# Optimization experiments

Hardware: AMD Instinct MI355X
Metric: run time of the kernel (lower is better)

## Reference

```python
import jax, jax.numpy as jnp
import numpy as np

HEADS = 8
DIM_HEAD = 64


def setup_inputs() -> dict:
    key = jax.random.key(0)
    ks = jax.random.split(key, 5)
    B, N, C, coor = 2, 2048, 256, 3
    dim_inner = HEADS * DIM_HEAD  # 512
    # weight scale 1/16 ~ 1/sqrt(256) keeps softmax logits in a sane range
    w_scale = 1.0 / 16.0
    return {
        "x": jax.random.normal(ks[0], (B, N, C, coor), dtype=jnp.float32),
        "Wq": jax.random.normal(ks[1], (dim_inner, C), dtype=jnp.float32) * w_scale,
        "Wk": jax.random.normal(ks[2], (dim_inner, C), dtype=jnp.float32) * w_scale,
        "Wv": jax.random.normal(ks[3], (dim_inner, C), dtype=jnp.float32) * w_scale,
        "Wo": jax.random.normal(ks[4], (C, dim_inner), dtype=jnp.float32) * w_scale,
    }


def _split_heads(t, B, N, coor):
    # b n (h d) c -> b h n (d c)
    t = t.reshape(B, N, HEADS, DIM_HEAD, coor)
    t = t.transpose(0, 2, 1, 3, 4)
    return t.reshape(B, HEADS, N, DIM_HEAD * coor)


def reference(x, Wq, Wk, Wv, Wo):
    B, N, C, coor = x.shape
    # VNLinear: einsum('... i c, o i -> ... o c')
    q = jnp.einsum('bnic,oi->bnoc', x, Wq)
    k = jnp.einsum('bnic,oi->bnoc', x, Wk)
    v = jnp.einsum('bnic,oi->bnoc', x, Wv)
    q = _split_heads(q, B, N, coor)  # (B, H, N, d*c)
    k = _split_heads(k, B, N, coor)
    v = _split_heads(v, B, N, coor)
    scale = (DIM_HEAD * coor) ** -0.5
    sim = jnp.einsum('bhie,bhje->bhij', q, k) * scale  # (B, H, N, N)
    attn = jax.nn.softmax(sim, axis=-1)
    out = jnp.einsum('bhij,bhje->bhie', attn, v)  # (B, H, N, d*c)
    # b h n (d c) -> b n (h d) c
    out = out.reshape(B, HEADS, N, DIM_HEAD, coor).transpose(0, 2, 1, 3, 4)
    out = out.reshape(B, N, HEADS * DIM_HEAD, coor)
    # to_out VNLinear
    return jnp.einsum('bnic,oi->bnoc', out, Wo)  # (B, N, C, 3)
```

## Files before the change

### kernel.cpp

```cpp
#include <hip/hip_runtime.h>

#define HEADS 8
#define DH 64
#define CO 3
#define E 192
#define NSEQ 2048
#define BATCH 2
#define CIN 256
#define DINNER 512
#define NTOK 4096
#define BHTOT 16

typedef __attribute__((ext_vector_type(8))) short bf16x8;
typedef __attribute__((ext_vector_type(4))) short bf16x4;
typedef __attribute__((ext_vector_type(4))) float f32x4;

static __device__ inline short f2bf(float f) {
  union { float f; unsigned u; } v; v.f = f;
  unsigned r = (v.u + 0x7FFFu + ((v.u >> 16) & 1u)) >> 16;
  return (short)r;
}

static __device__ inline void load_lds16(const short* g, short* l) {
  __builtin_amdgcn_global_load_lds(
      (const __attribute__((address_space(1))) void*)g,
      (__attribute__((address_space(3))) void*)l, 16, 0, 0);
}


__global__ __launch_bounds__(256) void prep_w(const float* __restrict__ Wq,
                                              const float* __restrict__ Wk,
                                              const float* __restrict__ Wv,
                                              const float* __restrict__ Wo,
                                              short* __restrict__ wqkvp,
                                              short* __restrict__ wop) {
  int idx = blockIdx.x * 256 + threadIdx.x;
  const float qscale = 0.07216878364870323f * 1.4426950408889634f;
  if (idx < 1536 * 256) {
    int o = idx >> 8, i = idx & 255;
    float v;
    if (o < 512) v = Wq[idx] * qscale;
    else if (o < 1024) v = Wk[idx - 512 * 256];
    else v = Wv[idx - 1024 * 256];
    int nt = o >> 4, ln = o & 15, ks = i >> 5, qd = (i >> 3) & 3, j = i & 7;
    wqkvp[((size_t)(nt * 8 + ks)) * 512 + (qd * 16 + ln) * 8 + j] = f2bf(v);
  } else {
    int j0 = idx - 1536 * 256;
    if (j0 < 256 * 512) {
      int o2 = j0 >> 9, i = j0 & 511;
      int nt = o2 >> 4, ln = o2 & 15, ks = i >> 5, qd = (i >> 3) & 3, j = i & 7;
      wop[((size_t)(nt * 16 + ks)) * 512 + (qd * 16 + ln) * 8 + j] = f2bf(Wo[j0]);
    }
  }
}

__global__ __launch_bounds__(256) void prep_x(const float* __restrict__ x,
                                              short* __restrict__ xcp) {
  int idx = blockIdx.x * 256 + threadIdx.x;
  int t = idx >> 8, i = idx & 255;
  const float* p = x + (size_t)idx * 3;
  float a = p[0], b = p[1], c = p[2];
  int mt = t >> 4, ln = t & 15, ks = i >> 5, qd = (i >> 3) & 3, j = i & 7;
  size_t inner = (size_t)(qd * 16 + ln) * 8 + j;
  xcp[((size_t)(0 * 256 + mt) * 8 + ks) * 512 + inner] = f2bf(a);
  xcp[((size_t)(1 * 256 + mt) * 8 + ks) * 512 + inner] = f2bf(b);
  xcp[((size_t)(2 * 256 + mt) * 8 + ks) * 512 + inner] = f2bf(c);
}

__global__ __launch_bounds__(256) void qkv_gemm(const short* __restrict__ xcp,
                                                const short* __restrict__ wqkvp,
                                                short* __restrict__ qp,
                                                short* __restrict__ kp,
                                                short* __restrict__ vp) {
  __shared__ __align__(16) short pool[17408];
  int c = blockIdx.z, ntb = blockIdx.x, mtb = blockIdx.y;
  int tid = threadIdx.x, wave = tid >> 6, lane = tid & 63;
  int ln = lane & 15, quad = lane >> 4;
  int wm = wave >> 1, wn = wave & 1;

  const short* gA = xcp + ((size_t)(c * 256 + mtb * 8) * 8) * 512;
  const short* gB = wqkvp + ((size_t)(ntb * 8) * 8) * 512;

  f32x4 acc[4][4] = {};
#pragma unroll
  for (int i = 0; i < 2; i++) {
    int q = tid + 256 * i, mf = q >> 6, l = q & 63;
    load_lds16(gA + (size_t)(mf * 8) * 512 + l * 8, pool + q * 8);
    load_lds16(gB + (size_t)(mf * 8) * 512 + l * 8, pool + 8192 + q * 8);
  }
  for (int ks = 0; ks < 8; ks++) {
    int b = ks & 1;
    __syncthreads();
    if (ks < 7) {
#pragma unroll
      for (int i = 0; i < 2; i++) {
        int q = tid + 256 * i, mf = q >> 6, l = q & 63;
        load_lds16(gA + (size_t)(mf * 8 + ks + 1) * 512 + l * 8, pool + (b ^ 1) * 4096 + q * 8);
        load_lds16(gB + (size_t)(mf * 8 + ks + 1) * 512 + l * 8, pool + 8192 + (b ^ 1) * 4096 + q * 8);
      }
    }
    const short* As = pool + b * 4096;
    const short* Bs = pool + 8192 + b * 4096;
    bf16x8 af[4], bfr[4];
#pragma unroll
    for (int i = 0; i < 4; i++) af[i] = *(const bf16x8*)&As[(wm * 4 + i) * 512 + lane * 8];
#pragma unroll
    for (int j = 0; j < 4; j++) bfr[j] = *(const bf16x8*)&Bs[(wn * 4 + j) * 512 + lane * 8];
#pragma unroll
    for (int i = 0; i < 4; i++)
#pragma unroll
      for (int j = 0; j < 4; j++)
        acc[i][j] = __builtin_amdgcn_mfma_f32_16x16x32_bf16(af[i], bfr[j], acc[i][j], 0, 0, 0);
  }

  int mat = ntb >> 2;
  int b0 = mtb >> 4;
  if (mat < 2) {
    __syncthreads();
    short* tp = pool;
#pragma unroll
    for (int i = 0; i < 4; i++)
#pragma unroll
      for (int j = 0; j < 4; j++)
#pragma unroll
        for (int jj = 0; jj < 4; jj++)
          tp[(wm * 64 + i * 16 + quad * 4 + jj) * 136 + wn * 64 + j * 16 + ln] =
              f2bf(acc[i][j][jj]);
    __syncthreads();
    short* dst = (mat == 0) ? qp : kp;
    int h0 = (ntb & 3) * 2;
#pragma unroll
    for (int rep = 0; rep < 8; rep++) {
      int gi = rep * 256 + tid;
      int l2 = gi & 15, qd = (gi >> 4) & 3, nf2 = (gi >> 6) & 3,
          esp = (gi >> 8) & 1, hh = (gi >> 9) & 1, kt2 = gi >> 10;
      int tl = kt2 * 64 + nf2 * 16 + l2;
      bf16x8 val = *(const bf16x8*)&tp[tl * 136 + hh * 64 + (esp * 4 + qd) * 8];
      int bhx = b0 * 8 + h0 + hh;
      int kt = (mtb * 2 + kt2) & 31;
      int es = c * 2 + esp;
      size_t off = (((size_t)((bhx * 32 + kt) * 24) + es * 4 + nf2) * 64 +
                    (size_t)(qd * 16 + l2)) * 8;
      *(bf16x8*)(dst + off) = val;
    }
  } else {
#pragma unroll
    for (int i = 0; i < 4; i++) {
      int kt = (mtb * 2 + wm) & 31;
      int ks2 = (i >> 1) & 1;
      int qd2 = (i * 2 + (quad >> 1)) & 3;
#pragma unroll
      for (int j = 0; j < 4; j++) {
        int o = ntb * 128 + wn * 64 + j * 16 + ln;
        int oo = o & 511, h = oo >> 6, d = oo & 63;
        int ef = c * 4 + (d >> 4), l2v = d & 15;
        int bhx = b0 * 8 + h;
        size_t off = ((size_t)((bhx * 32 + kt) * 24 + ks2 * 12 + ef)) * 512 +
                     (qd2 * 16 + l2v) * 8 + (quad & 1) * 4;
        bf16x4 val = { f2bf(acc[i][j][0]), f2bf(acc[i][j][1]),
                       f2bf(acc[i][j][2]), f2bf(acc[i][j][3]) };
        *(bf16x4*)(vp + off) = val;
      }
    }
  }
}

__global__ __launch_bounds__(256, 2) void attn(const short* __restrict__ qp,
                                               const short* __restrict__ kp,
                                               const short* __restrict__ vp,
                                               short* __restrict__ opart,
                                               float* __restrict__ lpart) {
  __shared__ __align__(16) short pool[33792];
  int pair = blockIdx.x, qt = blockIdx.y;
  int bh = pair & 15, kh = pair >> 4;
  int tid = threadIdx.x, wave = tid >> 6, lane = tid & 63;
  int ln = lane & 15, quad = lane >> 4;
  short* Kl = pool;
  short* Vl = pool + 12288;
  short* Pl = pool + 24576;

  bf16x8 qf[2][6];
#pragma unroll
  for (int rg = 0; rg < 2; rg++) {
    int fi = wave * 2 + rg;
    const short* qb = qp +
        ((size_t)(bh * 32 + qt * 2 + (fi >> 2)) * 24 + (fi & 3)) * 512 + lane * 8;
#pragma unroll
    for (int es = 0; es < 6; es++) qf[rg][es] = *(const bf16x8*)(qb + es * 2048);
  }

  float l_r[2][4] = {};
  f32x4 acc[2][12] = {};
  const short* gKb = kp + (size_t)(bh * 32 + kh * 16) * 12288;
  const short* gVb = vp + (size_t)(bh * 32 + kh * 16) * 12288;

  for (int kt = 0; kt < 16; kt++) {
    const short* gK = gKb + (size_t)kt * 12288;
    const short* gV = gVb + (size_t)kt * 12288;
#pragma unroll
    for (int i = 0; i < 6; i++) {
      load_lds16(gK + (i * 256 + tid) * 8, Kl + (i * 256 + tid) * 8);
      load_lds16(gV + (i * 256 + tid) * 8, Vl + (i * 256 + tid) * 8);
    }
    __syncthreads();

    f32x4 s[2][4];
#pragma unroll
    for (int nf = 0; nf < 4; nf++) {
      f32x4 a0 = {}, a1 = {};
#pragma unroll
      for (int es = 0; es < 6; es++) {
        bf16x8 kf = *(const bf16x8*)&Kl[(es * 4 + nf) * 512 + lane * 8];
        a0 = __builtin_amdgcn_mfma_f32_16x16x32_bf16(qf[0][es], kf, a0, 0, 0, 0);
        a1 = __builtin_amdgcn_mfma_f32_16x16x32_bf16(qf[1][es], kf, a1, 0, 0, 0);
      }
      s[0][nf] = a0; s[1][nf] = a1;
    }

#pragma unroll
    for (int rg = 0; rg < 2; rg++)
#pragma unroll
      for (int jj = 0; jj < 4; jj++)
#pragma unroll
        for (int nf = 0; nf < 4; nf++) {
          float p = __builtin_amdgcn_exp2f(s[rg][nf][jj]);
          union { float f; unsigned u; } v; v.f = p;
          Pl[((wave * 2 + rg) * 16 + quad * 4 + jj) * 72 + nf * 16 + ln] =
              (short)((v.u + 0x8000u) >> 16);
          l_r[rg][jj] += p;
        }

    bf16x8 pa[2][2];
#pragma unroll
    for (int rg = 0; rg < 2; rg++) {
      const short* pb = &Pl[((wave * 2 + rg) * 16 + ln) * 72 + quad * 8];
      pa[rg][0] = *(const bf16x8*)pb;
      pa[rg][1] = *(const bf16x8*)(pb + 32);
    }
#pragma unroll
    for (int ef = 0; ef < 12; ef++) {
      bf16x8 v0 = *(const bf16x8*)&Vl[ef * 512 + lane * 8];
      bf16x8 v1 = *(const bf16x8*)&Vl[(12 + ef) * 512 + lane * 8];
#pragma unroll
      for (int rg = 0; rg < 2; rg++) {
        acc[rg][ef] = __builtin_amdgcn_mfma_f32_16x16x32_bf16(pa[rg][0], v0, acc[rg][ef], 0, 0, 0);
        acc[rg][ef] = __builtin_amdgcn_mfma_f32_16x16x32_bf16(pa[rg][1], v1, acc[rg][ef], 0, 0, 0);
      }
    }
    __syncthreads();
  }

#pragma unroll
  for (int rg = 0; rg < 2; rg++)
#pragma unroll
    for (int jj = 0; jj < 4; jj++)
#pragma unroll
      for (int off = 1; off < 16; off <<= 1)
        l_r[rg][jj] += __shfl_xor(l_r[rg][jj], off, 64);

  short* tp = pool;
#pragma unroll
  for (int rg = 0; rg < 2; rg++)
#pragma unroll
    for (int jj = 0; jj < 4; jj++) {
      int row = (wave * 2 + rg) * 16 + quad * 4 + jj;
#pragma unroll
      for (int ef = 0; ef < 12; ef++)
        tp[row * 200 + ef * 16 + ln] = f2bf(acc[rg][ef][jj]);
    }
  __syncthreads();
  const size_t obase = ((size_t)(kh * 16 + bh) * 2048 + qt * 128) * 192;
#pragma unroll
  for (int rep = 0; rep < 12; rep++) {
    int gi = rep * 256 + tid;
    int row = gi / 24, c8 = gi - row * 24;
    *(bf16x8*)(opart + obase + (size_t)row * 192 + c8 * 8) =
        *(const bf16x8*)&tp[row * 200 + c8 * 8];
  }
  int lb = (kh * 16 + bh) * 2048 + qt * 128;
  if (ln == 0) {
#pragma unroll
    for (int rg = 0; rg < 2; rg++)
#pragma unroll
      for (int jj = 0; jj < 4; jj++)
        lpart[lb + (wave * 2 + rg) * 16 + quad * 4 + jj] = l_r[rg][jj];
  }
}

__global__ __launch_bounds__(256) void merge(const short* __restrict__ opart,
                                             const float* __restrict__ lpart,
                                             short* __restrict__ owp) {
  int G = blockIdx.x * 256 + threadIdx.x;
  int inner = G & 63, qd = inner >> 4, row16 = inner & 15;
  int ks = (G >> 6) & 15, h = ks >> 1, esp = ks & 1;
  int mt = (G >> 10) & 255;
  int c = G >> 18;
  int t = mt * 16 + row16, b = t >> 11, n = t & 2047;
  int bh = b * 8 + h;
  size_t so = ((size_t)bh * 2048 + n) * 192 + c * 64 + esp * 32 + qd * 8;
  const size_t HSTR = (size_t)16 * 2048 * 192;
  bf16x8 o1 = *(const bf16x8*)(opart + so);
  bf16x8 o2 = *(const bf16x8*)(opart + HSTR + so);
  float l = lpart[bh * 2048 + n] + lpart[16 * 2048 + bh * 2048 + n];
  float inv = 1.f / l;
  bf16x8 r;
#pragma unroll
  for (int j = 0; j < 8; j++) {
    union { unsigned u; float f; } a, b2;
    a.u = ((unsigned)(unsigned short)o1[j]) << 16;
    b2.u = ((unsigned)(unsigned short)o2[j]) << 16;
    r[j] = f2bf((a.f + b2.f) * inv);
  }
  *(bf16x8*)(owp + (size_t)G * 8) = r;
}

__global__ __launch_bounds__(256) void out_gemm(const short* __restrict__ owp,
                                                const short* __restrict__ wop,
                                                float* __restrict__ out) {
  __shared__ __align__(16) short Al[4096], Bl[2048];
  int c = blockIdx.z, ntb = blockIdx.x, mtb = blockIdx.y;
  int tid = threadIdx.x, wave = tid >> 6, lane = tid & 63;
  int ln = lane & 15, quad = lane >> 4;
  int wm = wave >> 1, wn = wave & 1;

  f32x4 acc[4][2] = {};
  const short* gAb = owp + ((size_t)(c * 256 + mtb * 8) * 16) * 512;
  const short* gBb = wop + ((size_t)(ntb * 4) * 16) * 512;
  for (int ks = 0; ks < 16; ks++) {
#pragma unroll
    for (int i = 0; i < 2; i++) {
      int q = tid + 256 * i, mf = q >> 6, l = q & 63;
      load_lds16(gAb + (size_t)(mf * 16 + ks) * 512 + l * 8, &Al[q * 8]);
    }
    {
      int nf2 = tid >> 6;
      load_lds16(gBb + (size_t)(nf2 * 16 + ks) * 512 + lane * 8, &Bl[tid * 8]);
    }
    __syncthreads();
    bf16x8 af[4], bfr[2];
#pragma unroll
    for (int i = 0; i < 4; i++) af[i] = *(const bf16x8*)&Al[(wm * 4 + i) * 512 + lane * 8];
#pragma unroll
    for (int j = 0; j < 2; j++) bfr[j] = *(const bf16x8*)&Bl[(wn * 2 + j) * 512 + lane * 8];
#pragma unroll
    for (int i = 0; i < 4; i++)
#pragma unroll
      for (int j = 0; j < 2; j++)
        acc[i][j] = __builtin_amdgcn_mfma_f32_16x16x32_bf16(af[i], bfr[j], acc[i][j], 0, 0, 0);
    __syncthreads();
  }
#pragma unroll
  for (int i = 0; i < 4; i++) {
#pragma unroll
    for (int j = 0; j < 2; j++) {
      int o2 = ntb * 64 + (wn * 2 + j) * 16 + ln;
#pragma unroll
      for (int jj = 0; jj < 4; jj++) {
        int t = mtb * 128 + (wm * 4 + i) * 16 + quad * 4 + jj;
        out[((size_t)t * 256 + o2) * 3 + c] = acc[i][j][jj];
      }
    }
  }
}

extern "C" void kernel_launch(void* const* d_in, const int* in_sizes, int n_in,
                              void* d_out, int out_size, void* d_ws, size_t ws_size,
                              hipStream_t stream) {
  const float* x  = (const float*)d_in[0];
  const float* Wq = (const float*)d_in[1];
  const float* Wk = (const float*)d_in[2];
  const float* Wv = (const float*)d_in[3];
  const float* Wo = (const float*)d_in[4];
  float* out = (float*)d_out;

  short* ws    = (short*)d_ws;
  short* xcp   = ws;
  short* wqkvp = xcp + 3 * NTOK * CIN;
  short* wop   = wqkvp + 1536 * 256;
  short* qp    = wop + 256 * 512;
  short* kp    = qp + (size_t)BHTOT * NSEQ * E;
  short* vp    = kp + (size_t)BHTOT * NSEQ * E;
  short* owp   = vp + (size_t)BHTOT * NSEQ * E;
  short* opart = owp + (size_t)3 * NTOK * DINNER;
  float* lpart = (float*)(opart + (size_t)2 * BHTOT * NSEQ * E);

  prep_w<<<2048, 256, 0, stream>>>(Wq, Wk, Wv, Wo, wqkvp, wop);
  prep_x<<<NTOK * CIN / 256, 256, 0, stream>>>(x, xcp);
  qkv_gemm<<<dim3(12, 32, 3), 256, 0, stream>>>(xcp, wqkvp, qp, kp, vp);
  attn<<<dim3(32, 16), 256, 0, stream>>>(qp, kp, vp, opart, lpart);
  merge<<<3072, 256, 0, stream>>>(opart, lpart, owp);
  out_gemm<<<dim3(4, 32, 3), 256, 0, stream>>>(owp, wop, out);
}
```

Measured before the change: 173.6 us.

## Fuse prep kernels, shrink out_gemm tiles, add launch bounds, alias workspace buffers

Merges the weight and input preparation kernels into one launch, which removes a kernel launch. Halves the out_gemm M tile so twice as many blocks run, and adds occupancy hints to qkv_gemm and out_gemm. Reuses workspace by placing lpart over xcp and owp over qp to shrink the memory footprint, which relies on those buffers being dead by the time they are overwritten. Smaller out_gemm tiles load the B operand more often relative to the compute they feed.

New measurement: 170.3 us. Within noise of the previous version (-1.9%).

```diff
diff --git a/kernel.cpp b/kernel.cpp
--- a/kernel.cpp
+++ b/kernel.cpp
@@ -28,13 +28,27 @@
 }
 
 
-__global__ __launch_bounds__(256) void prep_w(const float* __restrict__ Wq,
-                                              const float* __restrict__ Wk,
-                                              const float* __restrict__ Wv,
-                                              const float* __restrict__ Wo,
-                                              short* __restrict__ wqkvp,
-                                              short* __restrict__ wop) {
-  int idx = blockIdx.x * 256 + threadIdx.x;
+__global__ __launch_bounds__(256) void prep(const float* __restrict__ x,
+                                            const float* __restrict__ Wq,
+                                            const float* __restrict__ Wk,
+                                            const float* __restrict__ Wv,
+                                            const float* __restrict__ Wo,
+                                            short* __restrict__ xcp,
+                                            short* __restrict__ wqkvp,
+                                            short* __restrict__ wop) {
+  int gid = blockIdx.x * 256 + threadIdx.x;
+  if (gid < NTOK * CIN) {
+    int t = gid >> 8, i = gid & 255;
+    const float* p = x + (size_t)gid * 3;
+    float a = p[0], b = p[1], c = p[2];
+    int mt = t >> 4, ln = t & 15, ks = i >> 5, qd = (i >> 3) & 3, j = i & 7;
+    size_t inner = (size_t)(qd * 16 + ln) * 8 + j;
+    xcp[((size_t)(0 * 256 + mt) * 8 + ks) * 512 + inner] = f2bf(a);
+    xcp[((size_t)(1 * 256 + mt) * 8 + ks) * 512 + inner] = f2bf(b);
+    xcp[((size_t)(2 * 256 + mt) * 8 + ks) * 512 + inner] = f2bf(c);
+    return;
+  }
+  int idx = gid - NTOK * CIN;
   const float qscale = 0.07216878364870323f * 1.4426950408889634f;
   if (idx < 1536 * 256) {
     int o = idx >> 8, i = idx & 255;
@@ -54,24 +68,11 @@
   }
 }
 
-__global__ __launch_bounds__(256) void prep_x(const float* __restrict__ x,
-                                              short* __restrict__ xcp) {
-  int idx = blockIdx.x * 256 + threadIdx.x;
-  int t = idx >> 8, i = idx & 255;
-  const float* p = x + (size_t)idx * 3;
-  float a = p[0], b = p[1], c = p[2];
-  int mt = t >> 4, ln = t & 15, ks = i >> 5, qd = (i >> 3) & 3, j = i & 7;
-  size_t inner = (size_t)(qd * 16 + ln) * 8 + j;
-  xcp[((size_t)(0 * 256 + mt) * 8 + ks) * 512 + inner] = f2bf(a);
-  xcp[((size_t)(1 * 256 + mt) * 8 + ks) * 512 + inner] = f2bf(b);
-  xcp[((size_t)(2 * 256 + mt) * 8 + ks) * 512 + inner] = f2bf(c);
-}
-
-__global__ __launch_bounds__(256) void qkv_gemm(const short* __restrict__ xcp,
-                                                const short* __restrict__ wqkvp,
-                                                short* __restrict__ qp,
-                                                short* __restrict__ kp,
-                                                short* __restrict__ vp) {
+__global__ __launch_bounds__(256, 3) void qkv_gemm(const short* __restrict__ xcp,
+                                                   const short* __restrict__ wqkvp,
+                                                   short* __restrict__ qp,
+                                                   short* __restrict__ kp,
+                                                   short* __restrict__ vp) {
   __shared__ __align__(16) short pool[17408];
   int c = blockIdx.z, ntb = blockIdx.x, mtb = blockIdx.y;
   int tid = threadIdx.x, wave = tid >> 6, lane = tid & 63;
@@ -301,7 +302,7 @@
   const size_t HSTR = (size_t)16 * 2048 * 192;
   bf16x8 o1 = *(const bf16x8*)(opart + so);
   bf16x8 o2 = *(const bf16x8*)(opart + HSTR + so);
-  float l = lpart[bh * 2048 + n] + lpart[16 * 2048 + bh * 2048 + n];
+  float l = lpart[bh * 2048 + n] + lpart[32768 + bh * 2048 + n];
   float inv = 1.f / l;
   bf16x8 r;
 #pragma unroll
@@ -314,49 +315,45 @@
   *(bf16x8*)(owp + (size_t)G * 8) = r;
 }
 
-__global__ __launch_bounds__(256) void out_gemm(const short* __restrict__ owp,
-                                                const short* __restrict__ wop,
-                                                float* __restrict__ out) {
-  __shared__ __align__(16) short Al[4096], Bl[2048];
+__global__ __launch_bounds__(256, 4) void out_gemm(const short* __restrict__ owp,
+                                                   const short* __restrict__ wop,
+                                                   float* __restrict__ out) {
+  __shared__ __align__(16) short Al[2048], Bl[2048];
   int c = blockIdx.z, ntb = blockIdx.x, mtb = blockIdx.y;
   int tid = threadIdx.x, wave = tid >> 6, lane = tid & 63;
   int ln = lane & 15, quad = lane >> 4;
   int wm = wave >> 1, wn = wave & 1;
 
-  f32x4 acc[4][2] = {};
-  const short* gAb = owp + ((size_t)(c * 256 + mtb * 8) * 16) * 512;
+  f32x4 acc[2][2] = {};
+  const short* gAb = owp + ((size_t)(c * 256 + mtb * 4) * 16) * 512;
   const short* gBb = wop + ((size_t)(ntb * 4) * 16) * 512;
   for (int ks = 0; ks < 16; ks++) {
-#pragma unroll
-    for (int i = 0; i < 2; i++) {
-      int q = tid + 256 * i, mf = q >> 6, l = q & 63;
-      load_lds16(gAb + (size_t)(mf * 16 + ks) * 512 + l * 8, &Al[q * 8]);
-    }
     {
-      int nf2 = tid >> 6;
-      load_lds16(gBb + (size_t)(nf2 * 16 + ks) * 512 + lane * 8, &Bl[tid * 8]);
-    }
-    __syncthreads();
-    bf16x8 af[4], bfr[2];
-#pragma unroll
-    for (int i = 0; i < 4; i++) af[i] = *(const bf16x8*)&Al[(wm * 4 + i) * 512 + lane * 8];
+      int mf = tid >> 6, l = tid & 63;
+      load_lds16(gAb + (size_t)(mf * 16 + ks) * 512 + l * 8, &Al[tid * 8]);
+      load_lds16(gBb + (size_t)(mf * 16 + ks) * 512 + l * 8, &Bl[tid * 8]);
+    }
+    __syncthreads();
+    bf16x8 af[2], bfr[2];
+#pragma unroll
+    for (int i = 0; i < 2; i++) af[i] = *(const bf16x8*)&Al[(wm * 2 + i) * 512 + lane * 8];
 #pragma unroll
     for (int j = 0; j < 2; j++) bfr[j] = *(const bf16x8*)&Bl[(wn * 2 + j) * 512 + lane * 8];
 #pragma unroll
-    for (int i = 0; i < 4; i++)
+    for (int i = 0; i < 2; i++)
 #pragma unroll
       for (int j = 0; j < 2; j++)
         acc[i][j] = __builtin_amdgcn_mfma_f32_16x16x32_bf16(af[i], bfr[j], acc[i][j], 0, 0, 0);
     __syncthreads();
   }
 #pragma unroll
-  for (int i = 0; i < 4; i++) {
+  for (int i = 0; i < 2; i++) {
 #pragma unroll
     for (int j = 0; j < 2; j++) {
       int o2 = ntb * 64 + (wn * 2 + j) * 16 + ln;
 #pragma unroll
       for (int jj = 0; jj < 4; jj++) {
-        int t = mtb * 128 + (wm * 4 + i) * 16 + quad * 4 + jj;
+        int t = mtb * 64 + (wm * 2 + i) * 16 + quad * 4 + jj;
         out[((size_t)t * 256 + o2) * 3 + c] = acc[i][j][jj];
       }
     }
@@ -380,14 +377,13 @@
   short* qp    = wop + 256 * 512;
   short* kp    = qp + (size_t)BHTOT * NSEQ * E;
   short* vp    = kp + (size_t)BHTOT * NSEQ * E;
-  short* owp   = vp + (size_t)BHTOT * NSEQ * E;
-  short* opart = owp + (size_t)3 * NTOK * DINNER;
-  float* lpart = (float*)(opart + (size_t)2 * BHTOT * NSEQ * E);
-
-  prep_w<<<2048, 256, 0, stream>>>(Wq, Wk, Wv, Wo, wqkvp, wop);
-  prep_x<<<NTOK * CIN / 256, 256, 0, stream>>>(x, xcp);
+  short* opart = vp + (size_t)BHTOT * NSEQ * E;
+  float* lpart = (float*)xcp;
+  short* owp   = qp;
+
+  prep<<<6144, 256, 0, stream>>>(x, Wq, Wk, Wv, Wo, xcp, wqkvp, wop);
   qkv_gemm<<<dim3(12, 32, 3), 256, 0, stream>>>(xcp, wqkvp, qp, kp, vp);
   attn<<<dim3(32, 16), 256, 0, stream>>>(qp, kp, vp, opart, lpart);
   merge<<<3072, 256, 0, stream>>>(opart, lpart, owp);
-  out_gemm<<<dim3(4, 32, 3), 256, 0, stream>>>(owp, wop, out);
-}
+  out_gemm<<<dim3(4, 64, 3), 256, 0, stream>>>(owp, wop, out);
+}
```
